# Performance work log

Measured on AMD Instinct MI355X. Metric: run time of the kernel, lower is better.

Reference implementation:

```python
import jax, jax.numpy as jnp
import numpy as np
import math

D_MODEL = 512
DK = D_MODEL // 4      # per-head dim = 128
DH = D_MODEL // 8      # half-head dim = 64
BS, QL, SL = 4, 2048, 2048


def setup_inputs() -> dict:
    key = jax.random.key(0)
    ks = jax.random.split(key, 16)
    h = D_MODEL // 2
    inp = {
        "q": jax.random.normal(ks[0], (2, BS, QL, h), jnp.float32),
        "k": jax.random.normal(ks[1], (2, BS, SL, h), jnp.float32),
        "v": jax.random.normal(ks[2], (2, BS, SL, h), jnp.float32),
        "q_spa_embed": jax.random.normal(ks[3], (BS, 1, DK, DK), jnp.float32) * 0.1,
        "kv_spa_embed": jax.random.normal(ks[4], (BS, SL, DK, DK), jnp.float32) * 0.1,
        "attention_bias": jax.random.normal(ks[5], (BS, SL), jnp.float32),
        "mask": jax.random.randint(ks[6], (BS, SL), 0, 2, jnp.int32),
        # Linear weights stored [in, out] (torch Linear(in,out).weight.T)
        "W_qa": jax.random.normal(ks[7], (h, h // 2), jnp.float32) / math.sqrt(h),
        "W_qb": jax.random.normal(ks[8], (h, h // 2), jnp.float32) / math.sqrt(h),
        "W_ka": jax.random.normal(ks[9], (h, h // 2), jnp.float32) / math.sqrt(h),
        "W_kb": jax.random.normal(ks[10], (h, h // 2), jnp.float32) / math.sqrt(h),
        "W_va": jax.random.normal(ks[11], (h, h // 2), jnp.float32) / math.sqrt(h),
        "W_vb": jax.random.normal(ks[12], (h, h // 2), jnp.float32) / math.sqrt(h),
        "W_oa": jax.random.normal(ks[13], (h, h), jnp.float32) / math.sqrt(h),
        "W_ob": jax.random.normal(ks[14], (h, h), jnp.float32) / math.sqrt(h),
    }
    return inp


def _make_heads(xa, xb):
    # xa, xb: [bs, L, d_model//4] -> [bs, 4, L, dk] with head pattern
    # (a0,b0),(a1,b0),(a0,b1),(a1,b1)
    bs, L, _ = xa.shape
    xa = xa.reshape(bs, L, 2, DH)
    xb = xb.reshape(bs, L, 2, DH)
    xa = jnp.tile(xa, (1, 1, 2, 1))            # [bs,L,4,DH]
    xb = jnp.repeat(xb, 2, axis=2)             # [bs,L,4,DH]
    return jnp.concatenate([xa, xb], axis=-1).transpose(0, 2, 1, 3)  # [bs,4,L,DK]


def reference(q, k, v, q_spa_embed, kv_spa_embed, attention_bias, mask,
              W_qa, W_qb, W_ka, W_kb, W_va, W_vb, W_oa, W_ob):
    bs, ql = q.shape[1], q.shape[2]
    sl = k.shape[2]
    qh = _make_heads(q[0] @ W_qa, q[1] @ W_qb)   # [bs,4,ql,DK]
    kh = _make_heads(k[0] @ W_ka, k[1] @ W_kb)   # [bs,4,sl,DK]
    vh = _make_heads(v[0] @ W_va, v[1] @ W_vb)   # [bs,4,sl,DK]

    # per-token spatial rotation (seq_len == kv_spa_embed.shape[1] branch)
    qh = jnp.einsum('bij,bhqj->bhqi', q_spa_embed[:, 0], qh)
    kh = jnp.einsum('bsij,bhsj->bhsi', kv_spa_embed, kh)

    scores = jnp.einsum('bhqd,bhsd->bhqs', qh, kh) / math.sqrt(D_MODEL // 4)
    scores = scores + mask.astype(scores.dtype)[:, None, None, :] * (-1e9)
    attn = jax.nn.softmax(scores - attention_bias[:, None, None, :], axis=-1)
    # dropout: identity (eval mode)
    out = jnp.einsum('bhqs,bhsd->bhqd', attn, vh)          # [bs,4,ql,DK]

    out = out.reshape(bs, 4, ql, 2, DH)
    oa = out[:, :, :, 0].transpose(0, 2, 1, 3).reshape(bs, ql, -1) @ W_oa
    ob = out[:, :, :, 1].transpose(0, 2, 1, 3).reshape(bs, ql, -1) @ W_ob
    return jnp.stack([oa, ob], axis=0), attn
```

## Files before the change

kernel.cpp:

```cpp
#include <hip/hip_runtime.h>
#include <math.h>

#define QL 2048
#define SL 2048
#define BS 4
#define NH 4
#define FSZ ((size_t)BS * QL * 128)

typedef short bf16x8 __attribute__((ext_vector_type(8)));
typedef float f32x4 __attribute__((ext_vector_type(4)));

__device__ __forceinline__ short to_bf16_rne(float x) {
    unsigned u = __float_as_uint(x);
    unsigned r = u + 0x7fffu + ((u >> 16) & 1u);
    return (short)(r >> 16);
}

__device__ __forceinline__ void split8(const float* x, bf16x8& hi, bf16x8& lo) {
    #pragma unroll
    for (int j = 0; j < 8; j++) {
        short hh = to_bf16_rne(x[j]);
        float hf = __uint_as_float(((unsigned)(unsigned short)hh) << 16);
        hi[j] = hh;
        lo[j] = to_bf16_rne(x[j] - hf);
    }
}

__global__ __launch_bounds__(256) void proj_mfma_kernel(
    const float* __restrict__ q, const float* __restrict__ k, const float* __restrict__ v,
    const float* __restrict__ Wqa, const float* __restrict__ Wqb,
    const float* __restrict__ Wka, const float* __restrict__ Wkb,
    const float* __restrict__ Wva, const float* __restrict__ Wvb,
    float* __restrict__ ws)
{
    int id = blockIdx.y;
    const float* X; const float* W;
    const size_t HALF = (size_t)BS * QL * 256;
    switch (id) {
      case 0: X = q;        W = Wqa; break;
      case 1: X = q + HALF; W = Wqb; break;
      case 2: X = k;        W = Wka; break;
      case 3: X = k + HALF; W = Wkb; break;
      case 4: X = v;        W = Wva; break;
      default:X = v + HALF; W = Wvb; break;
    }
    float* Y = ws + (size_t)id * FSZ;
    int m0 = blockIdx.x * 128;

    __shared__ short lA[128 * 64];
    __shared__ short lB[128 * 64];

    int t = threadIdx.x;
    int srow = t >> 1, shalf = t & 1;
    int l = t & 63, w = t >> 6;
    int wr = w >> 1, wc = w & 1;
    int lr = l & 15, kb = l >> 4;

    f32x4 acc[4][4] = {};

    for (int kc = 0; kc < 256; kc += 32) {
        {
            const float* srcA = X + (size_t)(m0 + srow) * 256 + kc + shalf * 16;
            float xa[16];
            #pragma unroll
            for (int j = 0; j < 4; j++)
                *(float4*)&xa[j * 4] = *(const float4*)(srcA + j * 4);
            bf16x8 h0, l0, h1, l1;
            split8(&xa[0], h0, l0);
            split8(&xa[8], h1, l1);
            int base = srow * 64, r7 = srow & 7;
            *(bf16x8*)&lA[base + (((4 * shalf + 0) ^ r7) * 8)] = h0;
            *(bf16x8*)&lA[base + (((4 * shalf + 1) ^ r7) * 8)] = l0;
            *(bf16x8*)&lA[base + (((4 * shalf + 2) ^ r7) * 8)] = h1;
            *(bf16x8*)&lA[base + (((4 * shalf + 3) ^ r7) * 8)] = l1;
        }
        {
            int ncol = srow;
            float xb[16];
            #pragma unroll
            for (int j = 0; j < 16; j++)
                xb[j] = W[(size_t)(kc + shalf * 16 + j) * 128 + ncol];
            bf16x8 h0, l0, h1, l1;
            split8(&xb[0], h0, l0);
            split8(&xb[8], h1, l1);
            int base = ncol * 64, r7 = ncol & 7;
            *(bf16x8*)&lB[base + (((4 * shalf + 0) ^ r7) * 8)] = h0;
            *(bf16x8*)&lB[base + (((4 * shalf + 1) ^ r7) * 8)] = l0;
            *(bf16x8*)&lB[base + (((4 * shalf + 2) ^ r7) * 8)] = h1;
            *(bf16x8*)&lB[base + (((4 * shalf + 3) ^ r7) * 8)] = l1;
        }
        __syncthreads();

        bf16x8 ah[4], al[4], bhv[4], blv[4];
        #pragma unroll
        for (int m = 0; m < 4; m++) {
            int r = wr * 64 + m * 16 + lr;
            int r7 = r & 7, base = r * 64;
            ah[m] = *(bf16x8*)&lA[base + (((2 * kb + 0) ^ r7) * 8)];
            al[m] = *(bf16x8*)&lA[base + (((2 * kb + 1) ^ r7) * 8)];
        }
        #pragma unroll
        for (int n = 0; n < 4; n++) {
            int r = wc * 64 + n * 16 + lr;
            int r7 = r & 7, base = r * 64;
            bhv[n] = *(bf16x8*)&lB[base + (((2 * kb + 0) ^ r7) * 8)];
            blv[n] = *(bf16x8*)&lB[base + (((2 * kb + 1) ^ r7) * 8)];
        }
        #pragma unroll
        for (int m = 0; m < 4; m++) {
            #pragma unroll
            for (int n = 0; n < 4; n++) {
                acc[m][n] = __builtin_amdgcn_mfma_f32_16x16x32_bf16(ah[m], bhv[n], acc[m][n], 0, 0, 0);
                acc[m][n] = __builtin_amdgcn_mfma_f32_16x16x32_bf16(ah[m], blv[n], acc[m][n], 0, 0, 0);
                acc[m][n] = __builtin_amdgcn_mfma_f32_16x16x32_bf16(al[m], bhv[n], acc[m][n], 0, 0, 0);
            }
        }
        __syncthreads();
    }

    #pragma unroll
    for (int n = 0; n < 4; n++) {
        int gcol = wc * 64 + n * 16 + lr;
        #pragma unroll
        for (int m = 0; m < 4; m++) {
            int grow = m0 + wr * 64 + m * 16 + kb * 4;
            float* dst = Y + (size_t)grow * 128 + gcol;
            f32x4 c = acc[m][n];
            dst[0 * 128] = c[0];
            dst[1 * 128] = c[1];
            dst[2 * 128] = c[2];
            dst[3 * 128] = c[3];
        }
    }
}

__global__ __launch_bounds__(256) void rot_split_kernel(
    const float* __restrict__ ha, const float* __restrict__ hb,
    const float* __restrict__ E0, int per_token,
    short* __restrict__ rotS)
{
    int tkn = blockIdx.x;
    int b = blockIdx.y;
    const float* E = E0 + (per_token ? ((size_t)(b * SL + tkn) * 16384)
                                     : ((size_t)b * 16384));
    __shared__ float hv[4][128];
    __shared__ float outl[4][128];
    int tid = threadIdx.x;
    size_t tok = (size_t)(b * QL + tkn) * 128;
    for (int idx = tid; idx < 512; idx += 256) {
        int h = idx >> 7, d = idx & 127;
        float val = (d < 64) ? ha[tok + (h & 1) * 64 + d]
                             : hb[tok + (h >> 1) * 64 + (d - 64)];
        hv[h][d] = val;
    }
    __syncthreads();
    int w = tid >> 6, lane = tid & 63;
    int half = lane >> 5, l5 = lane & 31;
    for (int it = 0; it < 16; ++it) {
        int i = w * 32 + it * 2 + half;
        float4 e = *(const float4*)(E + (size_t)i * 128 + l5 * 4);
        float acc[4];
        #pragma unroll
        for (int h = 0; h < 4; h++) {
            float4 x = *(const float4*)&hv[h][l5 * 4];
            acc[h] = e.x * x.x + e.y * x.y + e.z * x.z + e.w * x.w;
        }
        #pragma unroll
        for (int off = 1; off < 32; off <<= 1) {
            #pragma unroll
            for (int h = 0; h < 4; h++) acc[h] += __shfl_xor(acc[h], off);
        }
        if (l5 < 4) outl[l5][i] = acc[l5];
    }
    __syncthreads();
    if (tid < 128) {
        int h    = tid >> 5;
        int kcid = (tid >> 3) & 3;
        int s    = tid & 7;
        int shalf = s >> 2;
        int isLo  = s & 1;
        int jbase = ((s >> 1) & 1) * 8;
        int dbase = kcid * 32 + shalf * 16 + jbase;
        bf16x8 outv;
        #pragma unroll
        for (int j = 0; j < 8; j++) {
            float x = outl[h][dbase + j];
            short hh = to_bf16_rne(x);
            if (isLo) {
                float hf = __uint_as_float(((unsigned)(unsigned short)hh) << 16);
                outv[j] = to_bf16_rne(x - hf);
            } else {
                outv[j] = hh;
            }
        }
        int bh = b * NH + h;
        int row = tkn & 127;
        size_t base = ((((size_t)bh * 16 + (tkn >> 7)) * 4 + kcid) * 128 + row) * 64;
        *(bf16x8*)&rotS[base + (size_t)((s ^ (row & 7)) * 8)] = outv;
    }
}

__global__ __launch_bounds__(256) void score_mfma_kernel(
    const short* __restrict__ qrotS, const short* __restrict__ krotS,
    const float* __restrict__ bias, const int* __restrict__ mask,
    float* __restrict__ attn, float* __restrict__ stats)
{
    __shared__ short lA[128 * 64];
    __shared__ short lB[128 * 64];
    __shared__ float redM[128][2];
    __shared__ float redS[128][2];

    int bid = blockIdx.x;
    int wg = (bid & 7) * 512 + (bid >> 3);
    int bh = wg >> 8;
    int qt = (wg >> 4) & 15, st = wg & 15;
    int q0 = qt * 128, s0 = st * 128;
    int b = bh >> 2;

    int t = threadIdx.x;
    int l = t & 63, w = t >> 6;
    int wr = w >> 1, wc = w & 1;
    int lr = l & 15, kb = l >> 4;

    const short* Abase = qrotS + (((size_t)bh * 16 + qt) * 4) * 8192;
    const short* Bbase = krotS + (((size_t)bh * 16 + st) * 4) * 8192;

    f32x4 acc[4][4] = {};

    for (int kcid = 0; kcid < 4; kcid++) {
        {
            const bf16x8* srcA = (const bf16x8*)(Abase + (size_t)kcid * 8192) + t * 4;
            const bf16x8* srcB = (const bf16x8*)(Bbase + (size_t)kcid * 8192) + t * 4;
            bf16x8 a0 = srcA[0], a1 = srcA[1], a2 = srcA[2], a3 = srcA[3];
            bf16x8 b0 = srcB[0], b1 = srcB[1], b2 = srcB[2], b3 = srcB[3];
            bf16x8* dA = (bf16x8*)lA + t * 4;
            bf16x8* dB = (bf16x8*)lB + t * 4;
            dA[0] = a0; dA[1] = a1; dA[2] = a2; dA[3] = a3;
            dB[0] = b0; dB[1] = b1; dB[2] = b2; dB[3] = b3;
        }
        __syncthreads();

        bf16x8 ah[4], al[4], bhv[4], blv[4];
        #pragma unroll
        for (int m = 0; m < 4; m++) {
            int r = wr * 64 + m * 16 + lr;
            int r7 = r & 7, base = r * 64;
            ah[m] = *(bf16x8*)&lA[base + (((2 * kb + 0) ^ r7) * 8)];
            al[m] = *(bf16x8*)&lA[base + (((2 * kb + 1) ^ r7) * 8)];
        }
        #pragma unroll
        for (int n = 0; n < 4; n++) {
            int r = wc * 64 + n * 16 + lr;
            int r7 = r & 7, base = r * 64;
            bhv[n] = *(bf16x8*)&lB[base + (((2 * kb + 0) ^ r7) * 8)];
            blv[n] = *(bf16x8*)&lB[base + (((2 * kb + 1) ^ r7) * 8)];
        }
        #pragma unroll
        for (int m = 0; m < 4; m++) {
            #pragma unroll
            for (int n = 0; n < 4; n++) {
                acc[m][n] = __builtin_amdgcn_mfma_f32_16x16x32_bf16(ah[m], bhv[n], acc[m][n], 0, 0, 0);
                acc[m][n] = __builtin_amdgcn_mfma_f32_16x16x32_bf16(ah[m], blv[n], acc[m][n], 0, 0, 0);
                acc[m][n] = __builtin_amdgcn_mfma_f32_16x16x32_bf16(al[m], bhv[n], acc[m][n], 0, 0, 0);
            }
        }
        __syncthreads();
    }

    const float scale = 0.08838834764831845f;
    #pragma unroll
    for (int n = 0; n < 4; n++) {
        int gs = s0 + wc * 64 + n * 16 + lr;
        float adj = -1e9f * (float)mask[b * SL + gs] - bias[b * SL + gs];
        #pragma unroll
        for (int m = 0; m < 4; m++) {
            int gq = q0 + wr * 64 + m * 16 + kb * 4;
            float* dst = attn + ((size_t)bh * QL + gq) * SL + gs;
            f32x4 c = acc[m][n];
            c[0] = c[0] * scale + adj;
            c[1] = c[1] * scale + adj;
            c[2] = c[2] * scale + adj;
            c[3] = c[3] * scale + adj;
            acc[m][n] = c;
            dst[0 * SL] = c[0];
            dst[1 * SL] = c[1];
            dst[2 * SL] = c[2];
            dst[3 * SL] = c[3];
        }
    }

    #pragma unroll
    for (int m = 0; m < 4; m++) {
        #pragma unroll
        for (int i = 0; i < 4; i++) {
            float rm = fmaxf(fmaxf(acc[m][0][i], acc[m][1][i]),
                             fmaxf(acc[m][2][i], acc[m][3][i]));
            rm = fmaxf(rm, __shfl_xor(rm, 1));
            rm = fmaxf(rm, __shfl_xor(rm, 2));
            rm = fmaxf(rm, __shfl_xor(rm, 4));
            rm = fmaxf(rm, __shfl_xor(rm, 8));
            if (lr == 0) redM[wr * 64 + m * 16 + kb * 4 + i][wc] = rm;
        }
    }
    __syncthreads();
    #pragma unroll
    for (int m = 0; m < 4; m++) {
        #pragma unroll
        for (int i = 0; i < 4; i++) {
            int row = wr * 64 + m * 16 + kb * 4 + i;
            float mt = fmaxf(redM[row][0], redM[row][1]);
            float es = __expf(acc[m][0][i] - mt) + __expf(acc[m][1][i] - mt)
                     + __expf(acc[m][2][i] - mt) + __expf(acc[m][3][i] - mt);
            es += __shfl_xor(es, 1);
            es += __shfl_xor(es, 2);
            es += __shfl_xor(es, 4);
            es += __shfl_xor(es, 8);
            if (lr == 0) redS[row][wc] = es;
        }
    }
    __syncthreads();
    if (t < 128) {
        float mt = fmaxf(redM[t][0], redM[t][1]);
        float es = redS[t][0] + redS[t][1];
        size_t r = (size_t)bh * QL + q0 + t;
        stats[(r * 16 + st) * 2 + 0] = mt;
        stats[(r * 16 + st) * 2 + 1] = es;
    }
}

__global__ __launch_bounds__(256) void sreduce_kernel(
    const float* __restrict__ stats,
    float* __restrict__ rowm, float* __restrict__ rowinv)
{
    int r = blockIdx.x * 256 + threadIdx.x;
    const float* src = stats + (size_t)r * 32;
    float4 p[8];
    #pragma unroll
    for (int j = 0; j < 8; j++) p[j] = *(const float4*)(src + j * 4);
    float m = -INFINITY;
    #pragma unroll
    for (int j = 0; j < 8; j++) { m = fmaxf(m, p[j].x); m = fmaxf(m, p[j].z); }
    float s = 0.f;
    #pragma unroll
    for (int j = 0; j < 8; j++) {
        s += p[j].y * __expf(p[j].x - m);
        s += p[j].w * __expf(p[j].z - m);
    }
    rowm[r] = m;
    rowinv[r] = 1.0f / s;
}

__global__ __launch_bounds__(256) void vtrans_kernel(
    const float* __restrict__ va, const float* __restrict__ vb,
    short* __restrict__ vT)
{
    int sblk = blockIdx.x;
    int bh = blockIdx.y;
    int b = bh >> 2, h = bh & 3;
    int hao = (h & 1) * 64, hbo = (h >> 1) * 64;
    __shared__ float vt[32][132];
    int t = threadIdx.x;
    for (int f = t; f < 1024; f += 256) {
        int s = f >> 5, c4 = (f & 31) * 4;
        size_t tok = (size_t)(b * SL + sblk * 32 + s) * 128;
        float4 vv = (c4 < 64) ? *(const float4*)(va + tok + hao + c4)
                              : *(const float4*)(vb + tok + hbo + (c4 - 64));
        *(float4*)&vt[s][c4] = vv;
    }
    __syncthreads();
    int d = t >> 1, shalf = t & 1;
    bf16x8 hi[2], lo[2];
    #pragma unroll
    for (int kb2 = 0; kb2 < 2; kb2++) {
        int kb = shalf * 2 + kb2;
        #pragma unroll
        for (int j = 0; j < 8; j++) {
            float x = vt[kb * 8 + j][d];
            short hh = to_bf16_rne(x);
            float hf = __uint_as_float(((unsigned)(unsigned short)hh) << 16);
            hi[kb2][j] = hh;
            lo[kb2][j] = to_bf16_rne(x - hf);
        }
    }
    size_t base = (((size_t)bh * 64 + sblk) * 128 + d) * 64;
    int d7 = d & 7;
    *(bf16x8*)&vT[base + (size_t)(((2 * (shalf * 2 + 0) + 0) ^ d7) * 8)] = hi[0];
    *(bf16x8*)&vT[base + (size_t)(((2 * (shalf * 2 + 0) + 1) ^ d7) * 8)] = lo[0];
    *(bf16x8*)&vT[base + (size_t)(((2 * (shalf * 2 + 1) + 0) ^ d7) * 8)] = hi[1];
    *(bf16x8*)&vT[base + (size_t)(((2 * (shalf * 2 + 1) + 1) ^ d7) * 8)] = lo[1];
}

__global__ __launch_bounds__(256) void pv_fused_kernel(
    float* __restrict__ attn, const short* __restrict__ vT,
    const float* __restrict__ rowm, const float* __restrict__ rowinv,
    float* __restrict__ outh)
{
    __shared__ short lA[128 * 64];
    __shared__ short lB[128 * 64];

    int bid = blockIdx.x;
    int wg = (bid & 7) * 32 + (bid >> 3);
    int bh = wg >> 4, qt = wg & 15;
    int q0 = qt * 128;

    float* Ag = attn + ((size_t)bh * QL + q0) * SL;
    const short* Bg = vT + (size_t)bh * 64 * 8192;

    int t = threadIdx.x;
    int srow = t >> 1, shalf = t & 1;
    int l = t & 63, w = t >> 6;
    int wr = w >> 1, wc = w & 1;
    int lr = l & 15, kb = l >> 4;

    float rm  = rowm[(size_t)bh * QL + q0 + srow];
    float riv = rowinv[(size_t)bh * QL + q0 + srow];

    f32x4 acc[4][4] = {};

    for (int sblk = 0; sblk < 64; sblk++) {
        {
            float* src = Ag + (size_t)srow * SL + sblk * 32 + shalf * 16;
            float x[16];
            #pragma unroll
            for (int j = 0; j < 4; j++)
                *(float4*)&x[j * 4] = *(const float4*)(src + j * 4);
            #pragma unroll
            for (int j = 0; j < 16; j++)
                x[j] = __expf(x[j] - rm) * riv;
            #pragma unroll
            for (int j = 0; j < 4; j++)
                *(float4*)(src + j * 4) = *(float4*)&x[j * 4];
            bf16x8 h0, l0, h1, l1;
            split8(&x[0], h0, l0);
            split8(&x[8], h1, l1);
            int base = srow * 64, r7 = srow & 7;
            *(bf16x8*)&lA[base + (((4 * shalf + 0) ^ r7) * 8)] = h0;
            *(bf16x8*)&lA[base + (((4 * shalf + 1) ^ r7) * 8)] = l0;
            *(bf16x8*)&lA[base + (((4 * shalf + 2) ^ r7) * 8)] = h1;
            *(bf16x8*)&lA[base + (((4 * shalf + 3) ^ r7) * 8)] = l1;
        }
        {
            const bf16x8* src = (const bf16x8*)(Bg + (size_t)sblk * 8192) + t * 4;
            bf16x8 v0 = src[0], v1 = src[1], v2 = src[2], v3 = src[3];
            bf16x8* dst = (bf16x8*)lB + t * 4;
            dst[0] = v0; dst[1] = v1; dst[2] = v2; dst[3] = v3;
        }
        __syncthreads();

        bf16x8 ah[4], al[4], bhv[4], blv[4];
        #pragma unroll
        for (int m = 0; m < 4; m++) {
            int r = wr * 64 + m * 16 + lr;
            int r7 = r & 7, base = r * 64;
            ah[m] = *(bf16x8*)&lA[base + (((2 * kb + 0) ^ r7) * 8)];
            al[m] = *(bf16x8*)&lA[base + (((2 * kb + 1) ^ r7) * 8)];
        }
        #pragma unroll
        for (int n = 0; n < 4; n++) {
            int r = wc * 64 + n * 16 + lr;
            int r7 = r & 7, base = r * 64;
            bhv[n] = *(bf16x8*)&lB[base + (((2 * kb + 0) ^ r7) * 8)];
            blv[n] = *(bf16x8*)&lB[base + (((2 * kb + 1) ^ r7) * 8)];
        }
        #pragma unroll
        for (int m = 0; m < 4; m++) {
            #pragma unroll
            for (int n = 0; n < 4; n++) {
                acc[m][n] = __builtin_amdgcn_mfma_f32_16x16x32_bf16(ah[m], bhv[n], acc[m][n], 0, 0, 0);
                acc[m][n] = __builtin_amdgcn_mfma_f32_16x16x32_bf16(ah[m], blv[n], acc[m][n], 0, 0, 0);
                acc[m][n] = __builtin_amdgcn_mfma_f32_16x16x32_bf16(al[m], bhv[n], acc[m][n], 0, 0, 0);
            }
        }
        __syncthreads();
    }

    #pragma unroll
    for (int n = 0; n < 4; n++) {
        int gd = wc * 64 + n * 16 + lr;
        #pragma unroll
        for (int m = 0; m < 4; m++) {
            int gq = q0 + wr * 64 + m * 16 + kb * 4;
            float* dst = outh + ((size_t)bh * QL + gq) * 128 + gd;
            f32x4 c = acc[m][n];
            dst[0 * 128] = c[0];
            dst[1 * 128] = c[1];
            dst[2 * 128] = c[2];
            dst[3 * 128] = c[3];
        }
    }
}

__global__ __launch_bounds__(256) void oproj_mfma_kernel(
    const float* __restrict__ outh, const float* __restrict__ Woa, const float* __restrict__ Wob,
    float* __restrict__ outp)
{
    int bt = blockIdx.x;
    int b = bt >> 4, tt = bt & 15;
    int t0 = tt * 128;
    int n0 = blockIdx.y * 128;
    int sel = blockIdx.z;
    const float* W = sel ? Wob : Woa;
    int doff = sel ? 64 : 0;

    __shared__ short lA[128 * 64];
    __shared__ short lB[128 * 64];

    int t = threadIdx.x;
    int srow = t >> 1, shalf = t & 1;
    int l = t & 63, w = t >> 6;
    int wr = w >> 1, wc = w & 1;
    int lr = l & 15, kb = l >> 4;

    f32x4 acc[4][4] = {};

    for (int kc = 0; kc < 256; kc += 32) {
        {
            int k0 = kc + shalf * 16;
            int h = k0 >> 6, d0 = k0 & 63;
            const float* srcA = outh + ((size_t)(b * NH + h) * QL + t0 + srow) * 128 + doff + d0;
            float xa[16];
            #pragma unroll
            for (int j = 0; j < 4; j++)
                *(float4*)&xa[j * 4] = *(const float4*)(srcA + j * 4);
            bf16x8 h0, l0, h1, l1;
            split8(&xa[0], h0, l0);
            split8(&xa[8], h1, l1);
            int base = srow * 64, r7 = srow & 7;
            *(bf16x8*)&lA[base + (((4 * shalf + 0) ^ r7) * 8)] = h0;
            *(bf16x8*)&lA[base + (((4 * shalf + 1) ^ r7) * 8)] = l0;
            *(bf16x8*)&lA[base + (((4 * shalf + 2) ^ r7) * 8)] = h1;
            *(bf16x8*)&lA[base + (((4 * shalf + 3) ^ r7) * 8)] = l1;
        }
        {
            int ncol = srow;
            float xb[16];
            #pragma unroll
            for (int j = 0; j < 16; j++)
                xb[j] = W[(size_t)(kc + shalf * 16 + j) * 256 + n0 + ncol];
            bf16x8 h0, l0, h1, l1;
            split8(&xb[0], h0, l0);
            split8(&xb[8], h1, l1);
            int base = ncol * 64, r7 = ncol & 7;
            *(bf16x8*)&lB[base + (((4 * shalf + 0) ^ r7) * 8)] = h0;
            *(bf16x8*)&lB[base + (((4 * shalf + 1) ^ r7) * 8)] = l0;
            *(bf16x8*)&lB[base + (((4 * shalf + 2) ^ r7) * 8)] = h1;
            *(bf16x8*)&lB[base + (((4 * shalf + 3) ^ r7) * 8)] = l1;
        }
        __syncthreads();

        bf16x8 ah[4], al[4], bhv[4], blv[4];
        #pragma unroll
        for (int m = 0; m < 4; m++) {
            int r = wr * 64 + m * 16 + lr;
            int r7 = r & 7, base = r * 64;
            ah[m] = *(bf16x8*)&lA[base + (((2 * kb + 0) ^ r7) * 8)];
            al[m] = *(bf16x8*)&lA[base + (((2 * kb + 1) ^ r7) * 8)];
        }
        #pragma unroll
        for (int n = 0; n < 4; n++) {
            int r = wc * 64 + n * 16 + lr;
            int r7 = r & 7, base = r * 64;
            bhv[n] = *(bf16x8*)&lB[base + (((2 * kb + 0) ^ r7) * 8)];
            blv[n] = *(bf16x8*)&lB[base + (((2 * kb + 1) ^ r7) * 8)];
        }
        #pragma unroll
        for (int m = 0; m < 4; m++) {
            #pragma unroll
            for (int n = 0; n < 4; n++) {
                acc[m][n] = __builtin_amdgcn_mfma_f32_16x16x32_bf16(ah[m], bhv[n], acc[m][n], 0, 0, 0);
                acc[m][n] = __builtin_amdgcn_mfma_f32_16x16x32_bf16(ah[m], blv[n], acc[m][n], 0, 0, 0);
                acc[m][n] = __builtin_amdgcn_mfma_f32_16x16x32_bf16(al[m], bhv[n], acc[m][n], 0, 0, 0);
            }
        }
        __syncthreads();
    }

    #pragma unroll
    for (int n = 0; n < 4; n++) {
        int gcol = n0 + wc * 64 + n * 16 + lr;
        #pragma unroll
        for (int m = 0; m < 4; m++) {
            int grow = t0 + wr * 64 + m * 16 + kb * 4;
            float* dst = outp + ((size_t)((sel * BS + b) * QL) + grow) * 256 + gcol;
            f32x4 c = acc[m][n];
            dst[0 * 256] = c[0];
            dst[1 * 256] = c[1];
            dst[2 * 256] = c[2];
            dst[3 * 256] = c[3];
        }
    }
}

extern "C" void kernel_launch(void* const* d_in, const int* in_sizes, int n_in,
                              void* d_out, int out_size, void* d_ws, size_t ws_size,
                              hipStream_t stream)
{
    const float* q    = (const float*)d_in[0];
    const float* k    = (const float*)d_in[1];
    const float* v    = (const float*)d_in[2];
    const float* qse  = (const float*)d_in[3];
    const float* kvse = (const float*)d_in[4];
    const float* bias = (const float*)d_in[5];
    const int*   mask = (const int*)d_in[6];
    const float* Wqa  = (const float*)d_in[7];
    const float* Wqb  = (const float*)d_in[8];
    const float* Wka  = (const float*)d_in[9];
    const float* Wkb  = (const float*)d_in[10];
    const float* Wva  = (const float*)d_in[11];
    const float* Wvb  = (const float*)d_in[12];
    const float* Woa  = (const float*)d_in[13];
    const float* Wob  = (const float*)d_in[14];

    float* outp = (float*)d_out;
    float* attn = outp + (size_t)2 * BS * QL * 256;

    float* ws     = (float*)d_ws;
    float* qa     = ws + 0 * FSZ;
    float* qb     = ws + 1 * FSZ;
    float* ka     = ws + 2 * FSZ;
    float* kb     = ws + 3 * FSZ;
    float* va     = ws + 4 * FSZ;
    float* vb     = ws + 5 * FSZ;
    short* qrotS  = (short*)(ws + 6 * FSZ);
    short* krotS  = (short*)(ws + 10 * FSZ);
    float* stats  = ws + 14 * FSZ;
    float* rowm   = ws + 15 * FSZ;
    float* rowinv = ws + 15 * FSZ + 32768;
    short* vT     = (short*)(ws + 16 * FSZ);
    float* outh   = ws + 20 * FSZ;

    proj_mfma_kernel<<<dim3(64, 6), 256, 0, stream>>>(q, k, v, Wqa, Wqb, Wka, Wkb, Wva, Wvb, ws);
    vtrans_kernel<<<dim3(64, 16), 256, 0, stream>>>(va, vb, vT);
    rot_split_kernel<<<dim3(QL, BS), 256, 0, stream>>>(qa, qb, qse, 0, qrotS);
    rot_split_kernel<<<dim3(SL, BS), 256, 0, stream>>>(ka, kb, kvse, 1, krotS);
    score_mfma_kernel<<<4096, 256, 0, stream>>>(qrotS, krotS, bias, mask, attn, stats);
    sreduce_kernel<<<128, 256, 0, stream>>>(stats, rowm, rowinv);
    pv_fused_kernel<<<256, 256, 0, stream>>>(attn, vT, rowm, rowinv, outh);
    oproj_mfma_kernel<<<dim3(64, 2, 2), 256, 0, stream>>>(outh, Woa, Wob, outp);
}
```

Measured before the change: 623.1 us.

## Use direct global-to-LDS loads in score and PV kernels; merge rotation launches

Replaces the register-staged global→LDS copies of the bf16 tiles in the score and PV kernels with the buffer/global load-to-LDS builtin, so tiles go straight into shared memory without passing through VGPRs. In the PV kernel the V-tile load is now issued before the softmax exponentiation work so it can overlap with that compute. The two rotation kernel launches for Q and K are merged into one grid that uses blockIdx.z to select Q or K, saving a launch. The direct-to-LDS path relies on the per-wave linear layout matching the previous copy layout, and it adds a dependency on correct vmcnt handling before the barrier.

```diff
diff --git a/kernel.cpp b/kernel.cpp
--- a/kernel.cpp
+++ b/kernel.cpp
@@ -135,14 +135,20 @@
 }
 
 __global__ __launch_bounds__(256) void rot_split_kernel(
-    const float* __restrict__ ha, const float* __restrict__ hb,
-    const float* __restrict__ E0, int per_token,
-    short* __restrict__ rotS)
+    const float* __restrict__ qa, const float* __restrict__ qb,
+    const float* __restrict__ ka, const float* __restrict__ kb,
+    const float* __restrict__ qse, const float* __restrict__ kvse,
+    short* __restrict__ qrotS, short* __restrict__ krotS)
 {
     int tkn = blockIdx.x;
     int b = blockIdx.y;
-    const float* E = E0 + (per_token ? ((size_t)(b * SL + tkn) * 16384)
-                                     : ((size_t)b * 16384));
+    int z = blockIdx.z;
+    const float* ha = z ? ka : qa;
+    const float* hb = z ? kb : qb;
+    const float* E = z ? (kvse + (size_t)(b * SL + tkn) * 16384)
+                       : (qse + (size_t)b * 16384);
+    short* rotS = z ? krotS : qrotS;
+
     __shared__ float hv[4][128];
     __shared__ float outl[4][128];
     int tid = threadIdx.x;
@@ -222,21 +228,25 @@
     int wr = w >> 1, wc = w & 1;
     int lr = l & 15, kb = l >> 4;
 
-    const short* Abase = qrotS + (((size_t)bh * 16 + qt) * 4) * 8192;
-    const short* Bbase = krotS + (((size_t)bh * 16 + st) * 4) * 8192;
+    const char* Abase = (const char*)(qrotS + (((size_t)bh * 16 + qt) * 4) * 8192);
+    const char* Bbase = (const char*)(krotS + (((size_t)bh * 16 + st) * 4) * 8192);
+    int lin = w * 4096 + l * 16;
 
     f32x4 acc[4][4] = {};
 
     for (int kcid = 0; kcid < 4; kcid++) {
         {
-            const bf16x8* srcA = (const bf16x8*)(Abase + (size_t)kcid * 8192) + t * 4;
-            const bf16x8* srcB = (const bf16x8*)(Bbase + (size_t)kcid * 8192) + t * 4;
-            bf16x8 a0 = srcA[0], a1 = srcA[1], a2 = srcA[2], a3 = srcA[3];
-            bf16x8 b0 = srcB[0], b1 = srcB[1], b2 = srcB[2], b3 = srcB[3];
-            bf16x8* dA = (bf16x8*)lA + t * 4;
-            bf16x8* dB = (bf16x8*)lB + t * 4;
-            dA[0] = a0; dA[1] = a1; dA[2] = a2; dA[3] = a3;
-            dB[0] = b0; dB[1] = b1; dB[2] = b2; dB[3] = b3;
+            const char* srcA = Abase + (size_t)kcid * 16384 + lin;
+            const char* srcB = Bbase + (size_t)kcid * 16384 + lin;
+            char* dA = (char*)lA + lin;
+            char* dB = (char*)lB + lin;
+            #pragma unroll
+            for (int j = 0; j < 4; j++) {
+                __builtin_amdgcn_global_load_lds((const unsigned int*)(srcA + j * 1024),
+                                                 (unsigned int*)(dA + j * 1024), 16, 0, 0);
+                __builtin_amdgcn_global_load_lds((const unsigned int*)(srcB + j * 1024),
+                                                 (unsigned int*)(dB + j * 1024), 16, 0, 0);
+            }
         }
         __syncthreads();
 
@@ -404,13 +414,14 @@
     int q0 = qt * 128;
 
     float* Ag = attn + ((size_t)bh * QL + q0) * SL;
-    const short* Bg = vT + (size_t)bh * 64 * 8192;
+    const char* Bg = (const char*)(vT + (size_t)bh * 64 * 8192);
 
     int t = threadIdx.x;
     int srow = t >> 1, shalf = t & 1;
     int l = t & 63, w = t >> 6;
     int wr = w >> 1, wc = w & 1;
     int lr = l & 15, kb = l >> 4;
+    int lin = w * 4096 + l * 16;
 
     float rm  = rowm[(size_t)bh * QL + q0 + srow];
     float riv = rowinv[(size_t)bh * QL + q0 + srow];
@@ -418,6 +429,15 @@
     f32x4 acc[4][4] = {};
 
     for (int sblk = 0; sblk < 64; sblk++) {
+        {
+            const char* srcB = Bg + (size_t)sblk * 16384 + lin;
+            char* dB = (char*)lB + lin;
+            #pragma unroll
+            for (int j = 0; j < 4; j++) {
+                __builtin_amdgcn_global_load_lds((const unsigned int*)(srcB + j * 1024),
+                                                 (unsigned int*)(dB + j * 1024), 16, 0, 0);
+            }
+        }
         {
             float* src = Ag + (size_t)srow * SL + sblk * 32 + shalf * 16;
             float x[16];
@@ -438,12 +458,6 @@
             *(bf16x8*)&lA[base + (((4 * shalf + 1) ^ r7) * 8)] = l0;
             *(bf16x8*)&lA[base + (((4 * shalf + 2) ^ r7) * 8)] = h1;
             *(bf16x8*)&lA[base + (((4 * shalf + 3) ^ r7) * 8)] = l1;
-        }
-        {
-            const bf16x8* src = (const bf16x8*)(Bg + (size_t)sblk * 8192) + t * 4;
-            bf16x8 v0 = src[0], v1 = src[1], v2 = src[2], v3 = src[3];
-            bf16x8* dst = (bf16x8*)lB + t * 4;
-            dst[0] = v0; dst[1] = v1; dst[2] = v2; dst[3] = v3;
         }
         __syncthreads();
 
@@ -631,8 +645,7 @@
 
     proj_mfma_kernel<<<dim3(64, 6), 256, 0, stream>>>(q, k, v, Wqa, Wqb, Wka, Wkb, Wva, Wvb, ws);
     vtrans_kernel<<<dim3(64, 16), 256, 0, stream>>>(va, vb, vT);
-    rot_split_kernel<<<dim3(QL, BS), 256, 0, stream>>>(qa, qb, qse, 0, qrotS);
-    rot_split_kernel<<<dim3(SL, BS), 256, 0, stream>>>(ka, kb, kvse, 1, krotS);
+    rot_split_kernel<<<dim3(QL, BS, 2), 256, 0, stream>>>(qa, qb, ka, kb, qse, kvse, qrotS, krotS);
     score_mfma_kernel<<<4096, 256, 0, stream>>>(qrotS, krotS, bias, mask, attn, stats);
     sreduce_kernel<<<128, 256, 0, stream>>>(stats, rowm, rowinv);
     pv_fused_kernel<<<256, 256, 0, stream>>>(attn, vT, rowm, rowinv, outh);
```

New measurement: 629.0 us. No clear change (+1.0%).
